# Kernel tuning notes

Hardware: AMD Instinct MI355X
Metric: run time of the kernel (lower is better)

Reference implementation:

```python
import jax, jax.numpy as jnp
import numpy as np

# Config constants (match init_kwargs / config)
B = 16        # config.BATCH_SIZE
T = 2048      # config.TRAIN_LEN
C = 256       # input channels (input_shape[-1])
K = 8         # kernel_size
F = 256       # nb_filters
DIL = 4       # dilation_rate


def setup_inputs() -> dict:
    key = jax.random.key(0)
    k1, k2, k3 = jax.random.split(key, 3)
    inputs = jax.random.normal(k1, (B, T, C), dtype=jnp.float32)
    kernel = jax.random.normal(k2, (C, K, F), dtype=jnp.float32) * 0.05
    bias = jax.random.normal(k3, (F,), dtype=jnp.float32) * 0.05
    return {"inputs": inputs, "kernel": kernel, "bias": bias}


def reference(inputs, kernel, bias):
    # Original TF layer computes, per (b,t,k,f):
    #   raw[b,t,k,f] = sum_c (x[b,t,c] * kernel[c,k,f] + bias[f])
    #               = conv[b,t,k,f] + C * bias[f]
    # (bias is added BEFORE the reduce_sum over the channel axis, so it is
    #  scaled by C — we reproduce that quirk faithfully.)
    # Then each (t,k) slice is scatter-added to output time t + k*dilation
    # (the gather_nd + zero-pad construction in TF implements exactly this
    #  dilated transposed-conv scatter; non-matching positions gather zeros),
    # and finally the last T timesteps are kept.
    Bq, Tq, Cq = inputs.shape
    Kq, Fq = kernel.shape[1], kernel.shape[2]
    conv = jnp.einsum('btc,ckf->btkf', inputs, kernel) + jnp.asarray(Cq, inputs.dtype) * bias
    L = Tq + (Kq - 1) * DIL  # final_time_len
    # scatter positions: out[i + j*DIL] += conv[:, i, j, :]
    pos = (jnp.arange(Tq)[:, None] + DIL * jnp.arange(Kq)[None, :]).reshape(-1)  # (T*K,)
    out = jnp.zeros((Bq, L, Fq), dtype=conv.dtype)
    out = out.at[:, pos, :].add(conv.reshape(Bq, Tq * Kq, Fq))
    return out[:, -Tq:, :]
```

## Files before the change

kernel.cpp:

```cpp
#include <hip/hip_runtime.h>
#include <hip/hip_bf16.h>


#define B_   16
#define T_   2048
#define C_   256
#define KT   8
#define F_   256
#define SH   28
#define BT   128
#define WIN  (BT + SH)
#define FB   19968
#define ABFB 9984
#define ABF  (2 * FB)

typedef __attribute__((ext_vector_type(8))) short short8;
typedef __attribute__((ext_vector_type(4))) float floatx4;
typedef __attribute__((ext_vector_type(4))) int   intx4;

__device__ inline void gload16(const void* g, void* l) {
    __builtin_amdgcn_global_load_lds(
        (const __attribute__((address_space(1))) void*)g,
        (__attribute__((address_space(3))) void*)l, 16, 0, 0);
}

__device__ inline short8 cvt8(float4 a, float4 b) {
    float v[8] = {a.x, a.y, a.z, a.w, b.x, b.y, b.z, b.w};
    short8 r;
    #pragma unroll
    for (int i = 0; i < 8; ++i) {
        __hip_bfloat16 h = __float2bfloat16(v[i]);
        r[i] = *reinterpret_cast<const short*>(&h);
    }
    return r;
}

__global__ __launch_bounds__(256) void wprep_kernel(const float* __restrict__ W,
                                                    ushort* __restrict__ Wf) {
    const int tid  = threadIdx.x;
    const int fid  = blockIdx.x * 4 + (tid >> 6);
    const int lane = tid & 63;
    const int g    = fid & 15;
    const int S    = fid >> 4;
    const int j    = S & 7, c = S >> 3;
    const int c0   = c * 32 + (lane >> 4) * 8;
    const int f    = g * 16 + (lane & 15);
    short8 pk;
    #pragma unroll
    for (int i = 0; i < 8; ++i) {
        __hip_bfloat16 h = __float2bfloat16(W[((c0 + i) * KT + j) * F_ + f]);
        pk[i] = *reinterpret_cast<const short*>(&h);
    }
    *reinterpret_cast<short8*>(Wf + (size_t)fid * 512 + lane * 8) = pk;
}

__global__ __launch_bounds__(256, 2) void deconv_kernel(
        const float* __restrict__ x, const ushort* __restrict__ Wf,
        const float* __restrict__ bias, float* __restrict__ out) {
    __shared__ alignas(16) char smem[59904];
    const int bid = blockIdx.x;
    const int fh  = bid & 1;
    const int tb  = bid >> 1;
    const int b   = tb & 15;
    const int t0  = (tb >> 4) * BT;
    const int tid = threadIdx.x;
    const int w   = tid >> 6, lane = tid & 63;
    const int l16 = lane & 15, q = lane >> 4;
    const int wm  = w >> 1, wf2 = w & 1;
    const char* wfbase = (const char*)Wf +
        (size_t)(fh * 8 + wf2 * 4) * 1024 + (size_t)lane * 16;

#define VMW(N_) do { asm volatile("s_waitcnt vmcnt(" #N_ ")" ::: "memory"); \
        __builtin_amdgcn_sched_barrier(0); } while (0)
#define LKW() do { asm volatile("s_waitcnt lgkmcnt(0)" ::: "memory");       \
        __builtin_amdgcn_sched_barrier(0); } while (0)
#define BAR() do { __builtin_amdgcn_sched_barrier(0);                       \
        __builtin_amdgcn_s_barrier();                                       \
        asm volatile("" ::: "memory");                                      \
        __builtin_amdgcn_sched_barrier(0); } while (0)

#define A_ROUND(k_, cc_) do {                                               \
        const int u_ = (k_) * 256 + tid;                                    \
        if ((k_) < 4 || tid < 224) {                                        \
            const int row_ = u_ >> 3, s_ = u_ & 7;                          \
            const int v_   = (s_ + 8 - (row_ & 7)) & 7;                     \
            int tr_ = t0 + row_; if (tr_ > T_ - 1) tr_ = T_ - 1;            \
            gload16(x + ((size_t)(b * T_ + tr_) * C_ + (cc_) * 32 + v_ * 4),\
                    smem + ((cc_) & 1) * FB + ((k_) * 256 + w * 64) * 16);  \
        } } while (0)

#define B_ISSUE(S_, sl_) do {                                               \
        const char* p_ = wfbase + (size_t)(S_) * 16384;                     \
        asm volatile("global_load_dwordx4 %0, %1, off"                      \
            : "=v"(bR[sl_][0]) : "v"(p_) : "memory");                       \
        asm volatile("global_load_dwordx4 %0, %1, off offset:1024"          \
            : "=v"(bR[sl_][1]) : "v"(p_) : "memory");                       \
        asm volatile("global_load_dwordx4 %0, %1, off offset:2048"          \
            : "=v"(bR[sl_][2]) : "v"(p_) : "memory");                       \
        asm volatile("global_load_dwordx4 %0, %1, off offset:3072"          \
            : "=v"(bR[sl_][3]) : "v"(p_) : "memory");                       \
        } while (0)

#define CVT_ROUND(r_, par_) do {                                            \
        if ((r_) < 2 || tid < 112) {                                        \
            const int task_ = (r_) * 256 + tid;                             \
            const int row_ = task_ >> 2, g_ = task_ & 3;                    \
            const int s1_ = (2 * g_ + row_) & 7;                            \
            const int s2_ = (2 * g_ + 1 + row_) & 7;                        \
            const char* fb_ = smem + (par_) * FB;                           \
            float4 u0_ = *(const float4*)(fb_ + (row_ * 8 + s1_) * 16);     \
            float4 u1_ = *(const float4*)(fb_ + (row_ * 8 + s2_) * 16);     \
            short8 pk_ = {0,0,0,0,0,0,0,0};                                 \
            if (t0 + row_ < T_) pk_ = cvt8(u0_, u1_);                       \
            const int p_ = g_ ^ ((row_ >> 1) & 3);                          \
            *(short8*)(smem + ABF + (par_) * ABFB + (row_ * 4 + p_) * 16)   \
                = pk_;                                                      \
        } } while (0)

#define MFMA_TAP(c_, j_) do {                                               \
        const char* ab_ = smem + ABF + ((c_) & 1) * ABFB;                   \
        short8 af_[4];                                                      \
        _Pragma("unroll")                                                   \
        for (int mf = 0; mf < 4; ++mf) {                                    \
            const int row_ = wm * 64 + (SH - 4 * (j_)) + mf * 16 + l16;     \
            const int p_   = q ^ ((row_ >> 1) & 3);                         \
            af_[mf] = *(const short8*)(ab_ + (row_ * 4 + p_) * 16);         \
        }                                                                   \
        __builtin_amdgcn_s_setprio(1);                                      \
        _Pragma("unroll")                                                   \
        for (int mf = 0; mf < 4; ++mf)                                      \
            _Pragma("unroll")                                               \
            for (int nf = 0; nf < 4; ++nf)                                  \
                acc[mf][nf] = __builtin_amdgcn_mfma_f32_16x16x32_bf16(      \
                    af_[mf],                                                \
                    *(short8*)&bR[(((c_) * 8 + (j_)) % 3)][nf],             \
                    acc[mf][nf], 0, 0, 0);                                  \
        __builtin_amdgcn_s_setprio(0);                                      \
        } while (0)

#define CHUNK_STD(c_) do {                                                  \
        A_ROUND(0, (c_)+1); A_ROUND(1, (c_)+1); A_ROUND(2, (c_)+1);         \
        A_ROUND(3, (c_)+1); A_ROUND(4, (c_)+1);                             \
        B_ISSUE((c_)*8+2, (((c_)*8+2)%3)); VMW(13); MFMA_TAP(c_, 0);        \
        B_ISSUE((c_)*8+3, (((c_)*8+3)%3)); VMW(13); MFMA_TAP(c_, 1);        \
        B_ISSUE((c_)*8+4, (((c_)*8+4)%3)); VMW(8);  MFMA_TAP(c_, 2);        \
        BAR();                                                              \
        B_ISSUE((c_)*8+5, (((c_)*8+5)%3)); VMW(8);  MFMA_TAP(c_, 3);        \
        B_ISSUE((c_)*8+6, (((c_)*8+6)%3)); VMW(8);  MFMA_TAP(c_, 4);        \
        B_ISSUE((c_)*8+7, (((c_)*8+7)%3)); VMW(8);  MFMA_TAP(c_, 5);        \
        CVT_ROUND(0, ((c_)+1)&1);                                           \
        B_ISSUE((c_)*8+8, (((c_)*8+8)%3)); VMW(8);  MFMA_TAP(c_, 6);        \
        CVT_ROUND(1, ((c_)+1)&1);                                           \
        B_ISSUE((c_)*8+9, (((c_)*8+9)%3)); VMW(8);  MFMA_TAP(c_, 7);        \
        CVT_ROUND(2, ((c_)+1)&1);                                           \
        LKW(); BAR();                                                       \
        } while (0)

    float bf4[4];
    #pragma unroll
    for (int nf = 0; nf < 4; ++nf)
        bf4[nf] = bias[fh * 128 + wf2 * 64 + nf * 16 + l16];

    floatx4 acc[4][4];
    #pragma unroll
    for (int mf = 0; mf < 4; ++mf)
        #pragma unroll
        for (int nf = 0; nf < 4; ++nf)
            acc[mf][nf] = (floatx4){0.f, 0.f, 0.f, 0.f};

    intx4 bR[3][4];

    A_ROUND(0, 0); A_ROUND(1, 0); A_ROUND(2, 0); A_ROUND(3, 0); A_ROUND(4, 0);
    B_ISSUE(0, 0); B_ISSUE(1, 1);
    VMW(8);
    BAR();
    CVT_ROUND(0, 0); CVT_ROUND(1, 0); CVT_ROUND(2, 0);
    LKW(); BAR();

    CHUNK_STD(0); CHUNK_STD(1); CHUNK_STD(2); CHUNK_STD(3);
    CHUNK_STD(4); CHUNK_STD(5); CHUNK_STD(6);

    B_ISSUE(58, (58 % 3)); VMW(8); MFMA_TAP(7, 0);
    B_ISSUE(59, (59 % 3)); VMW(8); MFMA_TAP(7, 1);
    B_ISSUE(60, (60 % 3)); VMW(8); MFMA_TAP(7, 2);
    B_ISSUE(61, (61 % 3)); VMW(8); MFMA_TAP(7, 3);
    B_ISSUE(62, (62 % 3)); VMW(8); MFMA_TAP(7, 4);
    B_ISSUE(63, (63 % 3)); VMW(8); MFMA_TAP(7, 5);
    VMW(4); MFMA_TAP(7, 6);
    VMW(0); MFMA_TAP(7, 7);

    #pragma unroll
    for (int mf = 0; mf < 4; ++mf) {
        #pragma unroll
        for (int nf = 0; nf < 4; ++nf) {
            const int f = fh * 128 + wf2 * 64 + nf * 16 + l16;
            #pragma unroll
            for (int r = 0; r < 4; ++r) {
                const int t = t0 + wm * 64 + mf * 16 + q * 4 + r;
                const int jmin = (t < T_ - SH) ? 0 : (((t - (T_ - SH)) >> 2) + 1);
                out[(size_t)(b * T_ + t) * F_ + f] =
                    acc[mf][nf][r] + (float)(8 - jmin) * 256.0f * bf4[nf];
            }
        }
    }
#undef VMW
#undef LKW
#undef BAR
#undef A_ROUND
#undef B_ISSUE
#undef CVT_ROUND
#undef MFMA_TAP
#undef CHUNK_STD
}

extern "C" void kernel_launch(void* const* d_in, const int* in_sizes, int n_in,
                              void* d_out, int out_size, void* d_ws, size_t ws_size,
                              hipStream_t stream) {
    const float* x    = (const float*)d_in[0];
    const float* W    = (const float*)d_in[1];
    const float* bias = (const float*)d_in[2];
    float* out = (float*)d_out;
    ushort* Wf = (ushort*)d_ws;

    wprep_kernel<<<256, 256, 0, stream>>>(W, Wf);
    deconv_kernel<<<512, 256, 0, stream>>>(x, Wf, bias, out);
}
```

Before: 44.24 us.

## Stage x through registers and hoist A fragments once per channel chunk

```diff
diff --git a/kernel.cpp b/kernel.cpp
--- a/kernel.cpp
+++ b/kernel.cpp
@@ -9,31 +9,13 @@
 #define F_   256
 #define SH   28
 #define BT   128
-#define WIN  (BT + SH)
-#define FB   19968
-#define ABFB 9984
-#define ABF  (2 * FB)
+#define WIN  156
+#define TPAD 192
+#define TILEB (TPAD * 64)
 
 typedef __attribute__((ext_vector_type(8))) short short8;
 typedef __attribute__((ext_vector_type(4))) float floatx4;
 typedef __attribute__((ext_vector_type(4))) int   intx4;
-
-__device__ inline void gload16(const void* g, void* l) {
-    __builtin_amdgcn_global_load_lds(
-        (const __attribute__((address_space(1))) void*)g,
-        (__attribute__((address_space(3))) void*)l, 16, 0, 0);
-}
-
-__device__ inline short8 cvt8(float4 a, float4 b) {
-    float v[8] = {a.x, a.y, a.z, a.w, b.x, b.y, b.z, b.w};
-    short8 r;
-    #pragma unroll
-    for (int i = 0; i < 8; ++i) {
-        __hip_bfloat16 h = __float2bfloat16(v[i]);
-        r[i] = *reinterpret_cast<const short*>(&h);
-    }
-    return r;
-}
 
 __global__ __launch_bounds__(256) void wprep_kernel(const float* __restrict__ W,
                                                     ushort* __restrict__ Wf) {
@@ -54,10 +36,25 @@
     *reinterpret_cast<short8*>(Wf + (size_t)fid * 512 + lane * 8) = pk;
 }
 
+__device__ inline short8 cvt8v(floatx4 a, floatx4 b) {
+    short8 r;
+    #pragma unroll
+    for (int i = 0; i < 4; ++i) {
+        __hip_bfloat16 h = __float2bfloat16(a[i]);
+        r[i] = *reinterpret_cast<const short*>(&h);
+    }
+    #pragma unroll
+    for (int i = 0; i < 4; ++i) {
+        __hip_bfloat16 h = __float2bfloat16(b[i]);
+        r[i + 4] = *reinterpret_cast<const short*>(&h);
+    }
+    return r;
+}
+
 __global__ __launch_bounds__(256, 2) void deconv_kernel(
         const float* __restrict__ x, const ushort* __restrict__ Wf,
         const float* __restrict__ bias, float* __restrict__ out) {
-    __shared__ alignas(16) char smem[59904];
+    __shared__ alignas(16) char smem[2 * TILEB];
     const int bid = blockIdx.x;
     const int fh  = bid & 1;
     const int tb  = bid >> 1;
@@ -69,6 +66,7 @@
     const int wm  = w >> 1, wf2 = w & 1;
     const char* wfbase = (const char*)Wf +
         (size_t)(fh * 8 + wf2 * 4) * 1024 + (size_t)lane * 16;
+    const int srow = tid >> 2, sg = tid & 3;
 
 #define VMW(N_) do { asm volatile("s_waitcnt vmcnt(" #N_ ")" ::: "memory"); \
         __builtin_amdgcn_sched_barrier(0); } while (0)
@@ -79,14 +77,36 @@
         asm volatile("" ::: "memory");                                      \
         __builtin_amdgcn_sched_barrier(0); } while (0)
 
-#define A_ROUND(k_, cc_) do {                                               \
-        const int u_ = (k_) * 256 + tid;                                    \
-        if ((k_) < 4 || tid < 224) {                                        \
-            const int row_ = u_ >> 3, s_ = u_ & 7;                          \
-            const int v_   = (s_ + 8 - (row_ & 7)) & 7;                     \
-            int tr_ = t0 + row_; if (tr_ > T_ - 1) tr_ = T_ - 1;            \
-            gload16(x + ((size_t)(b * T_ + tr_) * C_ + (cc_) * 32 + v_ * 4),\
-                    smem + ((cc_) & 1) * FB + ((k_) * 256 + w * 64) * 16);  \
+#define SL_ISSUE(cs_) do {                                                  \
+        _Pragma("unroll")                                                   \
+        for (int k = 0; k < 3; ++k) {                                       \
+            int tr_ = t0 + srow + 64 * k;                                   \
+            if (tr_ > T_ - 1) tr_ = T_ - 1;                                 \
+            const char* p_ = (const char*)(x +                              \
+                ((size_t)(b * T_ + tr_) * C_ + (cs_) * 32 + sg * 8));       \
+            asm volatile("global_load_dwordx4 %0, %1, off"                  \
+                : "=v"(sl[k][0]) : "v"(p_) : "memory");                     \
+            asm volatile("global_load_dwordx4 %0, %1, off offset:16"        \
+                : "=v"(sl[k][1]) : "v"(p_) : "memory");                     \
+        } } while (0)
+
+#define CVT_WRITE(buf_) do {                                                \
+        _Pragma("unroll")                                                   \
+        for (int k = 0; k < 3; ++k) {                                       \
+            const int row_ = srow + 64 * k;                                 \
+            short8 pk_ = {0,0,0,0,0,0,0,0};                                 \
+            if (t0 + row_ < T_) pk_ = cvt8v(sl[k][0], sl[k][1]);            \
+            const int p_ = sg ^ ((row_ >> 1) & 3);                          \
+            *(short8*)(smem + (buf_) * TILEB + row_ * 64 + p_ * 16) = pk_;  \
+        } } while (0)
+
+#define A_LOAD(buf_) do {                                                   \
+        _Pragma("unroll")                                                   \
+        for (int d = 0; d < 20; ++d) {                                      \
+            const int row_ = wm * 64 + l16 + 4 * d;                         \
+            const int p_   = q ^ ((row_ >> 1) & 3);                         \
+            a[d] = *(const short8*)(smem + (buf_) * TILEB +                 \
+                                    row_ * 64 + p_ * 16);                   \
         } } while (0)
 
 #define B_ISSUE(S_, sl_) do {                                               \
@@ -101,58 +121,39 @@
             : "=v"(bR[sl_][3]) : "v"(p_) : "memory");                       \
         } while (0)
 
-#define CVT_ROUND(r_, par_) do {                                            \
-        if ((r_) < 2 || tid < 112) {                                        \
-            const int task_ = (r_) * 256 + tid;                             \
-            const int row_ = task_ >> 2, g_ = task_ & 3;                    \
-            const int s1_ = (2 * g_ + row_) & 7;                            \
-            const int s2_ = (2 * g_ + 1 + row_) & 7;                        \
-            const char* fb_ = smem + (par_) * FB;                           \
-            float4 u0_ = *(const float4*)(fb_ + (row_ * 8 + s1_) * 16);     \
-            float4 u1_ = *(const float4*)(fb_ + (row_ * 8 + s2_) * 16);     \
-            short8 pk_ = {0,0,0,0,0,0,0,0};                                 \
-            if (t0 + row_ < T_) pk_ = cvt8(u0_, u1_);                       \
-            const int p_ = g_ ^ ((row_ >> 1) & 3);                          \
-            *(short8*)(smem + ABF + (par_) * ABFB + (row_ * 4 + p_) * 16)   \
-                = pk_;                                                      \
-        } } while (0)
-
-#define MFMA_TAP(c_, j_) do {                                               \
-        const char* ab_ = smem + ABF + ((c_) & 1) * ABFB;                   \
-        short8 af_[4];                                                      \
-        _Pragma("unroll")                                                   \
-        for (int mf = 0; mf < 4; ++mf) {                                    \
-            const int row_ = wm * 64 + (SH - 4 * (j_)) + mf * 16 + l16;     \
-            const int p_   = q ^ ((row_ >> 1) & 3);                         \
-            af_[mf] = *(const short8*)(ab_ + (row_ * 4 + p_) * 16);         \
-        }                                                                   \
+#define MFMA_TAP(j_, slot_) do {                                            \
         __builtin_amdgcn_s_setprio(1);                                      \
         _Pragma("unroll")                                                   \
         for (int mf = 0; mf < 4; ++mf)                                      \
             _Pragma("unroll")                                               \
             for (int nf = 0; nf < 4; ++nf)                                  \
                 acc[mf][nf] = __builtin_amdgcn_mfma_f32_16x16x32_bf16(      \
-                    af_[mf],                                                \
-                    *(short8*)&bR[(((c_) * 8 + (j_)) % 3)][nf],             \
+                    a[7 - (j_) + 4 * mf],                                   \
+                    *(short8*)&bR[slot_][nf],                               \
                     acc[mf][nf], 0, 0, 0);                                  \
         __builtin_amdgcn_s_setprio(0);                                      \
         } while (0)
 
-#define CHUNK_STD(c_) do {                                                  \
-        A_ROUND(0, (c_)+1); A_ROUND(1, (c_)+1); A_ROUND(2, (c_)+1);         \
-        A_ROUND(3, (c_)+1); A_ROUND(4, (c_)+1);                             \
-        B_ISSUE((c_)*8+2, (((c_)*8+2)%3)); VMW(13); MFMA_TAP(c_, 0);        \
-        B_ISSUE((c_)*8+3, (((c_)*8+3)%3)); VMW(13); MFMA_TAP(c_, 1);        \
-        B_ISSUE((c_)*8+4, (((c_)*8+4)%3)); VMW(8);  MFMA_TAP(c_, 2);        \
-        BAR();                                                              \
-        B_ISSUE((c_)*8+5, (((c_)*8+5)%3)); VMW(8);  MFMA_TAP(c_, 3);        \
-        B_ISSUE((c_)*8+6, (((c_)*8+6)%3)); VMW(8);  MFMA_TAP(c_, 4);        \
-        B_ISSUE((c_)*8+7, (((c_)*8+7)%3)); VMW(8);  MFMA_TAP(c_, 5);        \
-        CVT_ROUND(0, ((c_)+1)&1);                                           \
-        B_ISSUE((c_)*8+8, (((c_)*8+8)%3)); VMW(8);  MFMA_TAP(c_, 6);        \
-        CVT_ROUND(1, ((c_)+1)&1);                                           \
-        B_ISSUE((c_)*8+9, (((c_)*8+9)%3)); VMW(8);  MFMA_TAP(c_, 7);        \
-        CVT_ROUND(2, ((c_)+1)&1);                                           \
+#define CHUNK(c_) do {                                                      \
+        A_LOAD((c_) & 1);                                                   \
+        B_ISSUE((c_)*8+2, (((c_)*8+2)%3)); VMW(8);                          \
+        MFMA_TAP(0, (((c_)*8+0)%3));                                        \
+        B_ISSUE((c_)*8+3, (((c_)*8+3)%3)); VMW(8);                          \
+        MFMA_TAP(1, (((c_)*8+1)%3));                                        \
+        SL_ISSUE((c_) + 1);                                                 \
+        B_ISSUE((c_)*8+4, (((c_)*8+4)%3)); VMW(14);                         \
+        MFMA_TAP(2, (((c_)*8+2)%3));                                        \
+        B_ISSUE((c_)*8+5, (((c_)*8+5)%3)); VMW(14);                         \
+        MFMA_TAP(3, (((c_)*8+3)%3));                                        \
+        B_ISSUE((c_)*8+6, (((c_)*8+6)%3)); VMW(8);                          \
+        MFMA_TAP(4, (((c_)*8+4)%3));                                        \
+        B_ISSUE((c_)*8+7, (((c_)*8+7)%3)); VMW(8);                          \
+        MFMA_TAP(5, (((c_)*8+5)%3));                                        \
+        CVT_WRITE(((c_) + 1) & 1);                                          \
+        B_ISSUE((c_)*8+8, (((c_)*8+8)%3)); VMW(8);                          \
+        MFMA_TAP(6, (((c_)*8+6)%3));                                        \
+        B_ISSUE((c_)*8+9, (((c_)*8+9)%3)); VMW(8);                          \
+        MFMA_TAP(7, (((c_)*8+7)%3));                                        \
         LKW(); BAR();                                                       \
         } while (0)
 
@@ -168,26 +169,28 @@
         for (int nf = 0; nf < 4; ++nf)
             acc[mf][nf] = (floatx4){0.f, 0.f, 0.f, 0.f};
 
-    intx4 bR[3][4];
-
-    A_ROUND(0, 0); A_ROUND(1, 0); A_ROUND(2, 0); A_ROUND(3, 0); A_ROUND(4, 0);
+    short8  a[20];
+    intx4   bR[3][4];
+    floatx4 sl[3][2];
+
+    SL_ISSUE(0);
     B_ISSUE(0, 0); B_ISSUE(1, 1);
     VMW(8);
-    BAR();
-    CVT_ROUND(0, 0); CVT_ROUND(1, 0); CVT_ROUND(2, 0);
+    CVT_WRITE(0);
     LKW(); BAR();
 
-    CHUNK_STD(0); CHUNK_STD(1); CHUNK_STD(2); CHUNK_STD(3);
-    CHUNK_STD(4); CHUNK_STD(5); CHUNK_STD(6);
-
-    B_ISSUE(58, (58 % 3)); VMW(8); MFMA_TAP(7, 0);
-    B_ISSUE(59, (59 % 3)); VMW(8); MFMA_TAP(7, 1);
-    B_ISSUE(60, (60 % 3)); VMW(8); MFMA_TAP(7, 2);
-    B_ISSUE(61, (61 % 3)); VMW(8); MFMA_TAP(7, 3);
-    B_ISSUE(62, (62 % 3)); VMW(8); MFMA_TAP(7, 4);
-    B_ISSUE(63, (63 % 3)); VMW(8); MFMA_TAP(7, 5);
-    VMW(4); MFMA_TAP(7, 6);
-    VMW(0); MFMA_TAP(7, 7);
+    CHUNK(0); CHUNK(1); CHUNK(2); CHUNK(3);
+    CHUNK(4); CHUNK(5); CHUNK(6);
+
+    A_LOAD(1);
+    B_ISSUE(58, 1); VMW(8); MFMA_TAP(0, 2);
+    B_ISSUE(59, 2); VMW(8); MFMA_TAP(1, 0);
+    B_ISSUE(60, 0); VMW(8); MFMA_TAP(2, 1);
+    B_ISSUE(61, 1); VMW(8); MFMA_TAP(3, 2);
+    B_ISSUE(62, 2); VMW(8); MFMA_TAP(4, 0);
+    B_ISSUE(63, 0); VMW(8); MFMA_TAP(5, 1);
+    VMW(4); MFMA_TAP(6, 2);
+    VMW(0); MFMA_TAP(7, 0);
 
     #pragma unroll
     for (int mf = 0; mf < 4; ++mf) {
@@ -206,11 +209,12 @@
 #undef VMW
 #undef LKW
 #undef BAR
-#undef A_ROUND
+#undef SL_ISSUE
+#undef CVT_WRITE
+#undef A_LOAD
 #undef B_ISSUE
-#undef CVT_ROUND
 #undef MFMA_TAP
-#undef CHUNK_STD
+#undef CHUNK
 }
 
 extern "C" void kernel_launch(void* const* d_in, const int* in_sizes, int n_in,
```

New measurement: 49.85 us. +12.7%, slower.

## Prefetch A fragments into double-buffered registers and use a single fp32 staging buffer

Applied to the files above, without the earlier changes.

```diff
diff --git a/kernel.cpp b/kernel.cpp
--- a/kernel.cpp
+++ b/kernel.cpp
@@ -9,10 +9,10 @@
 #define F_   256
 #define SH   28
 #define BT   128
-#define WIN  (BT + SH)
+#define WIN  156
 #define FB   19968
+#define ABF  19968
 #define ABFB 9984
-#define ABF  (2 * FB)
 
 typedef __attribute__((ext_vector_type(8))) short short8;
 typedef __attribute__((ext_vector_type(4))) float floatx4;
@@ -57,7 +57,7 @@
 __global__ __launch_bounds__(256, 2) void deconv_kernel(
         const float* __restrict__ x, const ushort* __restrict__ Wf,
         const float* __restrict__ bias, float* __restrict__ out) {
-    __shared__ alignas(16) char smem[59904];
+    __shared__ alignas(16) char smem[39936];
     const int bid = blockIdx.x;
     const int fh  = bid & 1;
     const int tb  = bid >> 1;
@@ -86,7 +86,7 @@
             const int v_   = (s_ + 8 - (row_ & 7)) & 7;                     \
             int tr_ = t0 + row_; if (tr_ > T_ - 1) tr_ = T_ - 1;            \
             gload16(x + ((size_t)(b * T_ + tr_) * C_ + (cc_) * 32 + v_ * 4),\
-                    smem + ((cc_) & 1) * FB + ((k_) * 256 + w * 64) * 16);  \
+                    smem + ((k_) * 256 + w * 64) * 16);                     \
         } } while (0)
 
 #define B_ISSUE(S_, sl_) do {                                               \
@@ -107,9 +107,8 @@
             const int row_ = task_ >> 2, g_ = task_ & 3;                    \
             const int s1_ = (2 * g_ + row_) & 7;                            \
             const int s2_ = (2 * g_ + 1 + row_) & 7;                        \
-            const char* fb_ = smem + (par_) * FB;                           \
-            float4 u0_ = *(const float4*)(fb_ + (row_ * 8 + s1_) * 16);     \
-            float4 u1_ = *(const float4*)(fb_ + (row_ * 8 + s2_) * 16);     \
+            float4 u0_ = *(const float4*)(smem + (row_ * 8 + s1_) * 16);    \
+            float4 u1_ = *(const float4*)(smem + (row_ * 8 + s2_) * 16);    \
             short8 pk_ = {0,0,0,0,0,0,0,0};                                 \
             if (t0 + row_ < T_) pk_ = cvt8(u0_, u1_);                       \
             const int p_ = g_ ^ ((row_ >> 1) & 3);                          \
@@ -117,42 +116,58 @@
                 = pk_;                                                      \
         } } while (0)
 
-#define MFMA_TAP(c_, j_) do {                                               \
-        const char* ab_ = smem + ABF + ((c_) & 1) * ABFB;                   \
-        short8 af_[4];                                                      \
+#define LOAD_A(buf_, j_, arr) do {                                          \
+        const char* ab_ = smem + ABF + (buf_) * ABFB;                       \
         _Pragma("unroll")                                                   \
         for (int mf = 0; mf < 4; ++mf) {                                    \
             const int row_ = wm * 64 + (SH - 4 * (j_)) + mf * 16 + l16;     \
             const int p_   = q ^ ((row_ >> 1) & 3);                         \
-            af_[mf] = *(const short8*)(ab_ + (row_ * 4 + p_) * 16);         \
-        }                                                                   \
+            arr[mf] = *(const short8*)(ab_ + (row_ * 4 + p_) * 16);         \
+        } } while (0)
+
+#define MFMA_TAP(arr, slot_) do {                                           \
         __builtin_amdgcn_s_setprio(1);                                      \
         _Pragma("unroll")                                                   \
         for (int mf = 0; mf < 4; ++mf)                                      \
             _Pragma("unroll")                                               \
             for (int nf = 0; nf < 4; ++nf)                                  \
                 acc[mf][nf] = __builtin_amdgcn_mfma_f32_16x16x32_bf16(      \
-                    af_[mf],                                                \
-                    *(short8*)&bR[(((c_) * 8 + (j_)) % 3)][nf],             \
+                    arr[mf], *(short8*)&bR[slot_][nf],                      \
                     acc[mf][nf], 0, 0, 0);                                  \
         __builtin_amdgcn_s_setprio(0);                                      \
         } while (0)
 
-#define CHUNK_STD(c_) do {                                                  \
+#define CHUNK(c_) do {                                                      \
+        LOAD_A((c_) & 1, 0, a0);                                            \
         A_ROUND(0, (c_)+1); A_ROUND(1, (c_)+1); A_ROUND(2, (c_)+1);         \
         A_ROUND(3, (c_)+1); A_ROUND(4, (c_)+1);                             \
-        B_ISSUE((c_)*8+2, (((c_)*8+2)%3)); VMW(13); MFMA_TAP(c_, 0);        \
-        B_ISSUE((c_)*8+3, (((c_)*8+3)%3)); VMW(13); MFMA_TAP(c_, 1);        \
-        B_ISSUE((c_)*8+4, (((c_)*8+4)%3)); VMW(8);  MFMA_TAP(c_, 2);        \
+        LOAD_A((c_) & 1, 1, a1);                                            \
+        B_ISSUE((c_)*8+2, (((c_)*8+2)%3)); VMW(13);                         \
+        MFMA_TAP(a0, (((c_)*8+0)%3));                                       \
+        LOAD_A((c_) & 1, 2, a0);                                            \
+        B_ISSUE((c_)*8+3, (((c_)*8+3)%3)); VMW(13);                         \
+        MFMA_TAP(a1, (((c_)*8+1)%3));                                       \
+        LOAD_A((c_) & 1, 3, a1);                                            \
+        B_ISSUE((c_)*8+4, (((c_)*8+4)%3)); VMW(8);                          \
+        MFMA_TAP(a0, (((c_)*8+2)%3));                                       \
         BAR();                                                              \
-        B_ISSUE((c_)*8+5, (((c_)*8+5)%3)); VMW(8);  MFMA_TAP(c_, 3);        \
-        B_ISSUE((c_)*8+6, (((c_)*8+6)%3)); VMW(8);  MFMA_TAP(c_, 4);        \
-        B_ISSUE((c_)*8+7, (((c_)*8+7)%3)); VMW(8);  MFMA_TAP(c_, 5);        \
+        LOAD_A((c_) & 1, 4, a0);                                            \
+        B_ISSUE((c_)*8+5, (((c_)*8+5)%3)); VMW(8);                          \
+        MFMA_TAP(a1, (((c_)*8+3)%3));                                       \
+        LOAD_A((c_) & 1, 5, a1);                                            \
         CVT_ROUND(0, ((c_)+1)&1);                                           \
-        B_ISSUE((c_)*8+8, (((c_)*8+8)%3)); VMW(8);  MFMA_TAP(c_, 6);        \
+        B_ISSUE((c_)*8+6, (((c_)*8+6)%3)); VMW(8);                          \
+        MFMA_TAP(a0, (((c_)*8+4)%3));                                       \
+        LOAD_A((c_) & 1, 6, a0);                                            \
         CVT_ROUND(1, ((c_)+1)&1);                                           \
-        B_ISSUE((c_)*8+9, (((c_)*8+9)%3)); VMW(8);  MFMA_TAP(c_, 7);        \
+        B_ISSUE((c_)*8+7, (((c_)*8+7)%3)); VMW(8);                          \
+        MFMA_TAP(a1, (((c_)*8+5)%3));                                       \
+        LOAD_A((c_) & 1, 7, a1);                                            \
         CVT_ROUND(2, ((c_)+1)&1);                                           \
+        B_ISSUE((c_)*8+8, (((c_)*8+8)%3)); VMW(8);                          \
+        MFMA_TAP(a0, (((c_)*8+6)%3));                                       \
+        B_ISSUE((c_)*8+9, (((c_)*8+9)%3)); VMW(8);                          \
+        MFMA_TAP(a1, (((c_)*8+7)%3));                                       \
         LKW(); BAR();                                                       \
         } while (0)
 
@@ -168,7 +183,8 @@
         for (int nf = 0; nf < 4; ++nf)
             acc[mf][nf] = (floatx4){0.f, 0.f, 0.f, 0.f};
 
-    intx4 bR[3][4];
+    short8 a0[4], a1[4];
+    intx4  bR[3][4];
 
     A_ROUND(0, 0); A_ROUND(1, 0); A_ROUND(2, 0); A_ROUND(3, 0); A_ROUND(4, 0);
     B_ISSUE(0, 0); B_ISSUE(1, 1);
@@ -177,17 +193,19 @@
     CVT_ROUND(0, 0); CVT_ROUND(1, 0); CVT_ROUND(2, 0);
     LKW(); BAR();
 
-    CHUNK_STD(0); CHUNK_STD(1); CHUNK_STD(2); CHUNK_STD(3);
-    CHUNK_STD(4); CHUNK_STD(5); CHUNK_STD(6);
-
-    B_ISSUE(58, (58 % 3)); VMW(8); MFMA_TAP(7, 0);
-    B_ISSUE(59, (59 % 3)); VMW(8); MFMA_TAP(7, 1);
-    B_ISSUE(60, (60 % 3)); VMW(8); MFMA_TAP(7, 2);
-    B_ISSUE(61, (61 % 3)); VMW(8); MFMA_TAP(7, 3);
-    B_ISSUE(62, (62 % 3)); VMW(8); MFMA_TAP(7, 4);
-    B_ISSUE(63, (63 % 3)); VMW(8); MFMA_TAP(7, 5);
-    VMW(4); MFMA_TAP(7, 6);
-    VMW(0); MFMA_TAP(7, 7);
+    CHUNK(0); CHUNK(1); CHUNK(2); CHUNK(3);
+    CHUNK(4); CHUNK(5); CHUNK(6);
+
+    LOAD_A(1, 0, a0);
+    LOAD_A(1, 1, a1);
+    B_ISSUE(58, 1); VMW(8); MFMA_TAP(a0, 2); LOAD_A(1, 2, a0);
+    B_ISSUE(59, 2); VMW(8); MFMA_TAP(a1, 0); LOAD_A(1, 3, a1);
+    B_ISSUE(60, 0); VMW(8); MFMA_TAP(a0, 1); LOAD_A(1, 4, a0);
+    B_ISSUE(61, 1); VMW(8); MFMA_TAP(a1, 2); LOAD_A(1, 5, a1);
+    B_ISSUE(62, 2); VMW(8); MFMA_TAP(a0, 0); LOAD_A(1, 6, a0);
+    B_ISSUE(63, 0); VMW(8); MFMA_TAP(a1, 1); LOAD_A(1, 7, a1);
+    VMW(4); MFMA_TAP(a0, 2);
+    VMW(0); MFMA_TAP(a1, 0);
 
     #pragma unroll
     for (int mf = 0; mf < 4; ++mf) {
@@ -209,8 +227,9 @@
 #undef A_ROUND
 #undef B_ISSUE
 #undef CVT_ROUND
+#undef LOAD_A
 #undef MFMA_TAP
-#undef CHUNK_STD
+#undef CHUNK
 }
 
 extern "C" void kernel_launch(void* const* d_in, const int* in_sizes, int n_in,
```

After: 43.89 us. Within noise of the previous version (-0.8%).
